# Kernel optimization log

Measured on AMD Instinct MI355X. Metric: run time of the kernel, lower is better.

Reference implementation:

```python
import jax, jax.numpy as jnp
import numpy as np

NEG_FILL = -1e20
SPANS_PER_WORD = 2


def setup_inputs() -> dict:
    key = jax.random.key(0)
    k1, k2, k3, k4, k5 = jax.random.split(key, 5)
    B, N, D, T = 8, 16384, 256, 8
    embeddings = jax.random.normal(k1, (B, N, D), dtype=jnp.float32)
    scores_a = jax.random.normal(k2, (B, N, T), dtype=jnp.float32)
    scores_b = jax.random.normal(k3, (B, N, T), dtype=jnp.float32)
    span_mask = jax.random.randint(k4, (B, N), 0, 2).astype(bool)
    seq_length = jax.random.randint(k5, (B,), 1, 2048).astype(jnp.int32)
    return {
        "embeddings": embeddings,
        "scores_a": scores_a,
        "scores_b": scores_b,
        "span_mask": span_mask,
        "seq_length": seq_length,
    }


def reference(embeddings, scores_a, scores_b, span_mask, seq_length):
    # --- SpanPruner.forward: per-dict-entry softmax, drop null tag, max over tags ---
    probs_list = [jnp.max(jax.nn.softmax(s, axis=2)[:, :, 1:], axis=2)
                  for s in (scores_a, scores_b)]
    probabilities = jnp.maximum(probs_list[0], probs_list[1])  # max over dict entries  [B,N]

    # --- span_pruner ---
    num_keep = jnp.maximum(seq_length * SPANS_PER_WORD, 1)       # [B]
    max_keep = int(jnp.max(num_keep))                            # static k for topk

    scores = jnp.where(span_mask, probabilities, NEG_FILL)       # masked_fill  [B,N]
    _, top_indices = jax.lax.top_k(scores, max_keep)             # [B,K], descending like torch.topk

    top_indices_mask = jnp.arange(max_keep)[None, :] < num_keep[:, None]  # [B,K]
    fill_value = jnp.max(top_indices, axis=1, keepdims=True)
    top_indices = jnp.where(top_indices_mask, top_indices, fill_value)
    top_indices = jnp.sort(top_indices, axis=1)                  # [B,K]

    # batched_index_select gathers
    seq_mask = jnp.take_along_axis(span_mask, top_indices, axis=1)        # [B,K] bool
    top_mask = (top_indices_mask & seq_mask).astype(jnp.int32)            # [B,K]
    top_scores = jnp.take_along_axis(scores, top_indices, axis=1)         # [B,K]
    top_embeddings = jnp.take_along_axis(embeddings, top_indices[:, :, None], axis=1)  # [B,K,D]

    return top_indices, top_embeddings, top_scores, top_mask
```

## Files before the change

### kernel.cpp

```cpp
#include <hip/hip_runtime.h>
#include <math.h>

#define NB 8
#define NN 16384
#define NT 8
#define ND 256
#define NEG_FILL_F (-1e20f)

__device__ __forceinline__ unsigned fkey(float s){
  unsigned u = __float_as_uint(s);
  return (u & 0x80000000u) ? ~u : (u | 0x80000000u);
}
__device__ __forceinline__ float fkey_inv(unsigned k){
  unsigned u = (k & 0x80000000u) ? (k ^ 0x80000000u) : ~k;
  return __uint_as_float(u);
}

__device__ __forceinline__ float prob_of(const float4 x, const float4 y){
  float m = fmaxf(fmaxf(fmaxf(x.x,x.y),fmaxf(x.z,x.w)),
                  fmaxf(fmaxf(y.x,y.y),fmaxf(y.z,y.w)));
  float e0=expf(x.x-m), e1=expf(x.y-m), e2=expf(x.z-m), e3=expf(x.w-m);
  float e4=expf(y.x-m), e5=expf(y.y-m), e6=expf(y.z-m), e7=expf(y.w-m);
  float sum = ((((((e0+e1)+e2)+e3)+e4)+e5)+e6)+e7;
  float pm = fmaxf(fmaxf(fmaxf(e1,e2),fmaxf(e3,e4)),fmaxf(fmaxf(e5,e6),e7));
  return pm/sum;
}

__global__ void k_scores(const float* __restrict__ sa, const float* __restrict__ sb,
                         const int* __restrict__ mask, unsigned* __restrict__ outk,
                         int* __restrict__ gpart){
  __shared__ int lh[256];
  const int t = threadIdx.x;
  lh[t] = 0;
  __syncthreads();
  int i = blockIdx.x*256 + t;
  const float4* pa = (const float4*)(sa + (size_t)i*NT);
  const float4* pb = (const float4*)(sb + (size_t)i*NT);
  float4 a0=pa[0], a1=pa[1], b0=pb[0], b1=pb[1];
  float p = fmaxf(prob_of(a0,a1), prob_of(b0,b1));
  unsigned k = fkey(mask[i] ? p : NEG_FILL_F);
  outk[i] = k;
  atomicAdd(&lh[k>>24], 1);
  __syncthreads();
  gpart[blockIdx.x*256 + t] = lh[t];
}

__device__ int block_scan_excl(int v, int* lds, int tid){
  __syncthreads();
  int lane = tid & 63, wave = tid >> 6;
  int x = v;
  #pragma unroll
  for (int off=1; off<64; off<<=1){
    int y = __shfl_up(x, off, 64);
    if (lane >= off) x += y;
  }
  if (lane == 63) lds[wave] = x;
  __syncthreads();
  if (wave == 0){
    int w = (lane < 16) ? lds[lane] : 0;
    #pragma unroll
    for (int off=1; off<16; off<<=1){
      int y = __shfl_up(w, off, 64);
      if (lane >= off) w += y;
    }
    if (lane < 16) lds[16+lane] = w;
  }
  __syncthreads();
  int waveOff = wave ? lds[16+wave-1] : 0;
  return waveOff + x - v;
}

__device__ void build_hist(const unsigned* kk, unsigned pref, unsigned decided, int shift,
                           unsigned (*whist)[257], int* hist, int tid, int lane, int wave){
  #pragma unroll
  for (int i=0;i<4;++i) whist[wave][lane + 64*i] = 0u;
  __syncthreads();
  #pragma unroll
  for (int j=0;j<16;++j){
    unsigned k = kk[j];
    if (((k ^ pref) & decided) == 0u)
      atomicAdd(&whist[wave][(k>>shift)&255u], 1u);
  }
  __syncthreads();
  if (tid < 256){
    unsigned sum=0;
    #pragma unroll
    for (int w=0;w<16;++w) sum += whist[w][tid];
    hist[tid] = (int)sum;
  }
  __syncthreads();
}

__device__ void scan_pick2(int x, int r0, int r1, bool do1,
                           int* P, int* lds4, int* sOut, int tid, int lane, int wave){
  int Pt = 0;
  if (tid < 256){
    #pragma unroll
    for (int off=1; off<64; off<<=1){
      int y = __shfl_up(x, off, 64);
      if (lane >= off) x += y;
    }
    if (lane==63) lds4[wave] = x;
    Pt = x;
  }
  __syncthreads();
  if (tid < 256){
    int offs = 0;
    for (int w=0; w<wave; ++w) offs += lds4[w];
    Pt += offs;
    P[tid] = Pt;
  }
  __syncthreads();
  if (tid < 256){
    int prev = tid ? P[tid-1] : 0;
    if (Pt >= r0 && prev < r0){ sOut[0] = 255-tid; sOut[1] = r0-prev; }
    if (do1 && Pt >= r1 && prev < r1){ sOut[2] = 255-tid; sOut[3] = r1-prev; }
  }
  __syncthreads();
}

__global__ __launch_bounds__(1024)
void k_select(const unsigned* __restrict__ keys, const int* __restrict__ gpart,
              const int* __restrict__ seq, float* __restrict__ out, int K){
  const int b = blockIdx.x;
  const int tid = threadIdx.x;
  const int lane = tid & 63, wave = tid >> 6;
  __shared__ unsigned whist[16][257];
  __shared__ int part4[4][256];
  __shared__ int hist[256];
  __shared__ int P[256];
  __shared__ int lds[32];
  __shared__ int lds4[4];
  __shared__ int smax[16];
  __shared__ int sOut[4];
  __shared__ int sFill;

  int num_keep = seq[b]*2; if (num_keep < 1) num_keep = 1;

  {
    int grp = tid >> 8;
    int bin = tid & 255;
    const int* gp = gpart + (b*64 + grp*16)*256 + bin;
    int sum = 0;
    #pragma unroll
    for (int w=0; w<16; ++w) sum += gp[w*256];
    part4[grp][bin] = sum;
  }

  const unsigned* kb = keys + (size_t)b*NN + tid*16;
  unsigned kk[16];
  #pragma unroll
  for (int q=0;q<4;++q){
    uint4 v = ((const uint4*)kb)[q];
    kk[4*q+0]=v.x; kk[4*q+1]=v.y; kk[4*q+2]=v.z; kk[4*q+3]=v.w;
  }
  __syncthreads();

  int r0 = K, r1 = num_keep;
  int x0 = 0;
  if (tid < 256){
    int bin = 255 - tid;
    x0 = part4[0][bin] + part4[1][bin] + part4[2][bin] + part4[3][bin];
  }
  scan_pick2(x0, r0, r1, true, P, lds4, sOut, tid, lane, wave);
  unsigned pref0 = (unsigned)sOut[0] << 24;  r0 = sOut[1];
  unsigned pref1 = (unsigned)sOut[2] << 24;  r1 = sOut[3];
  bool same = (pref0 == pref1);
  unsigned decided = 0xFF000000u;
  __syncthreads();

  for (int round=1; round<4; ++round){
    const int shift = 24 - 8*round;
    build_hist(kk, pref0, decided, shift, whist, hist, tid, lane, wave);
    int xv = (tid < 256) ? hist[255-tid] : 0;
    scan_pick2(xv, r0, r1, same, P, lds4, sOut, tid, lane, wave);
    int bin0 = sOut[0], rem0 = sOut[1];
    int bin1 = sOut[2], rem1 = sOut[3];
    __syncthreads();
    if (!same){
      build_hist(kk, pref1, decided, shift, whist, hist, tid, lane, wave);
      int xv1 = (tid < 256) ? hist[255-tid] : 0;
      scan_pick2(xv1, r1, 0, false, P, lds4, sOut, tid, lane, wave);
      bin1 = sOut[0]; rem1 = sOut[1];
      __syncthreads();
    }
    pref0 |= (unsigned)bin0 << shift;  r0 = rem0;
    pref1 |= (unsigned)bin1 << shift;  r1 = rem1;
    same = same && (bin0 == bin1);
    decided |= (0xFFu << shift);
  }
  const unsigned TK = pref0;  const int needK = r0;
  const unsigned TN = pref1;  const int needN = r1;

  int cTK=0, cTN=0;
  #pragma unroll
  for (int j=0;j<16;++j){
    unsigned k = kk[j];
    cTK += (k==TK); cTN += (k==TN);
  }
  int oTK = block_scan_excl(cTK, lds, tid);
  int oTN = block_scan_excl(cTN, lds, tid);

  const int base = tid*16;
  int tK=oTK, tN=oTN, cKept=0, maxIdx=-1;
  #pragma unroll
  for (int j=0;j<16;++j){
    unsigned k=kk[j];
    bool inK  = (k>TK) || ((k==TK) && (tK<needK));  if (k==TK) tK++;
    bool kept = (k>TN) || ((k==TN) && (tN<needN));  if (k==TN) tN++;
    if (inK) maxIdx = base+j;
    cKept += kept;
  }
  int oKept = block_scan_excl(cKept, lds, tid);

  int mv=maxIdx;
  #pragma unroll
  for (int off=32; off; off>>=1){
    int y = __shfl_down(mv, off, 64);
    mv = mv > y ? mv : y;
  }
  if (lane==0) smax[wave]=mv;
  __syncthreads();
  if (tid==0){
    int f=-1;
    for (int i=0;i<16;++i) f = f > smax[i] ? f : smax[i];
    sFill = f;
  }
  __syncthreads();
  const int fill = sFill;

  float* out_idx = out;
  float* out_sc  = out + (size_t)NB*K + (size_t)NB*K*ND;
  float* out_mk  = out_sc + (size_t)NB*K;
  const int ob = b*K;
  const unsigned kNEG = fkey(NEG_FILL_F);

  int tN2=oTN, p=oKept;
  #pragma unroll
  for (int j=0;j<16;++j){
    unsigned k=kk[j];
    bool kept = (k>TN) || ((k==TN) && (tN2<needN));  if (k==TN) tN2++;
    if (kept){
      int n = base+j;
      out_idx[ob+p] = (float)n;
      out_sc[ob+p]  = fkey_inv(k);
      out_mk[ob+p]  = (k != kNEG) ? 1.0f : 0.0f;
      ++p;
    }
  }
  if (num_keep < K){
    float fs = fkey_inv(keys[(size_t)b*NN + fill]);
    for (int q = num_keep + tid; q < K; q += 1024){
      out_idx[ob+q] = (float)fill;
      out_sc[ob+q]  = fs;
      out_mk[ob+q]  = 0.0f;
    }
  }
}

__global__ void k_gather(const float* __restrict__ emb, const float* __restrict__ out_idx,
                         float* __restrict__ out_emb, int K){
  int b = blockIdx.y;
  int g = blockIdx.x*256 + threadIdx.x;
  if (g >= K*64) return;
  int c = g & 63;
  int p = g >> 6;
  size_t r = (size_t)b*K + p;
  int idx = (int)out_idx[r];
  const float4* src = (const float4*)(emb + ((size_t)b*NN + (size_t)idx)*ND);
  float4* dst = (float4*)(out_emb + r*(size_t)ND);
  dst[c] = src[c];
}

extern "C" void kernel_launch(void* const* d_in, const int* in_sizes, int n_in,
                              void* d_out, int out_size, void* d_ws, size_t ws_size,
                              hipStream_t stream) {
  const float* emb  = (const float*)d_in[0];
  const float* sa   = (const float*)d_in[1];
  const float* sb   = (const float*)d_in[2];
  const int*   mask = (const int*)d_in[3];
  const int*   seq  = (const int*)d_in[4];
  float* out = (float*)d_out;
  unsigned* ws_keys = (unsigned*)d_ws;
  int* gpart = (int*)d_ws + (size_t)NB*NN;

  int K = out_size / (NB*(ND+3));
  if (K <= 0) return;

  k_scores<<<(NB*NN)/256, 256, 0, stream>>>(sa, sb, mask, ws_keys, gpart);
  k_select<<<NB, 1024, 0, stream>>>(ws_keys, gpart, seq, out, K);
  dim3 ggrid((K*64 + 255)/256, NB);
  k_gather<<<ggrid, 256, 0, stream>>>(emb, out, out + (size_t)NB*K, K);
}
```

Baseline: 206.8 us.

## Halve select block size, fuse dual radix histograms and packed prefix scans

The per-batch top-k select kernel now runs 512 threads, each holding 32 keys, instead of 1024 threads holding 16. When the two radix thresholds diverge, both histograms are built in a single pass over the keys instead of two. The two exclusive scans for tie counts are packed into one 32-bit scan, and the cross-wave prefix is computed with a simple unrolled sum. Together these cut the number of barriers and LDS passes in a kernel launched with only 8 blocks, at the cost of more registers and less parallelism per block.

```diff
diff --git a/kernel.cpp b/kernel.cpp
--- a/kernel.cpp
+++ b/kernel.cpp
@@ -45,7 +45,7 @@
   gpart[blockIdx.x*256 + t] = lh[t];
 }
 
-__device__ int block_scan_excl(int v, int* lds, int tid){
+__device__ __forceinline__ int block_scan_excl512(int v, int* lds, int tid){
   __syncthreads();
   int lane = tid & 63, wave = tid >> 6;
   int x = v;
@@ -56,45 +56,18 @@
   }
   if (lane == 63) lds[wave] = x;
   __syncthreads();
-  if (wave == 0){
-    int w = (lane < 16) ? lds[lane] : 0;
-    #pragma unroll
-    for (int off=1; off<16; off<<=1){
-      int y = __shfl_up(w, off, 64);
-      if (lane >= off) w += y;
-    }
-    if (lane < 16) lds[16+lane] = w;
-  }
-  __syncthreads();
-  int waveOff = wave ? lds[16+wave-1] : 0;
-  return waveOff + x - v;
-}
-
-__device__ void build_hist(const unsigned* kk, unsigned pref, unsigned decided, int shift,
-                           unsigned (*whist)[257], int* hist, int tid, int lane, int wave){
-  #pragma unroll
-  for (int i=0;i<4;++i) whist[wave][lane + 64*i] = 0u;
-  __syncthreads();
-  #pragma unroll
-  for (int j=0;j<16;++j){
-    unsigned k = kk[j];
-    if (((k ^ pref) & decided) == 0u)
-      atomicAdd(&whist[wave][(k>>shift)&255u], 1u);
-  }
-  __syncthreads();
-  if (tid < 256){
-    unsigned sum=0;
-    #pragma unroll
-    for (int w=0;w<16;++w) sum += whist[w][tid];
-    hist[tid] = (int)sum;
-  }
-  __syncthreads();
-}
-
-__device__ void scan_pick2(int x, int r0, int r1, bool do1,
-                           int* P, int* lds4, int* sOut, int tid, int lane, int wave){
+  int wo = 0;
+  #pragma unroll
+  for (int w=0; w<8; ++w) wo += (w < wave) ? lds[w] : 0;
+  return wo + x - v;
+}
+
+__device__ void scan_pick(const int* hist, int r0, int r1, bool do1,
+                          int* P, int* lds4, int* sOut, int tid, int lane){
   int Pt = 0;
-  if (tid < 256){
+  const int wave = tid >> 6;
+  if (tid < 256){
+    int x = hist[255 - tid];
     #pragma unroll
     for (int off=1; off<64; off<<=1){
       int y = __shfl_up(x, off, 64);
@@ -105,9 +78,10 @@
   }
   __syncthreads();
   if (tid < 256){
-    int offs = 0;
-    for (int w=0; w<wave; ++w) offs += lds4[w];
-    Pt += offs;
+    int wo = 0;
+    #pragma unroll
+    for (int w=0; w<4; ++w) wo += (w < wave) ? lds4[w] : 0;
+    Pt += wo;
     P[tid] = Pt;
   }
   __syncthreads();
@@ -119,20 +93,22 @@
   __syncthreads();
 }
 
-__global__ __launch_bounds__(1024)
+__global__ __launch_bounds__(512, 1)
 void k_select(const unsigned* __restrict__ keys, const int* __restrict__ gpart,
               const int* __restrict__ seq, float* __restrict__ out, int K){
   const int b = blockIdx.x;
   const int tid = threadIdx.x;
   const int lane = tid & 63, wave = tid >> 6;
-  __shared__ unsigned whist[16][257];
-  __shared__ int part4[4][256];
-  __shared__ int hist[256];
+  __shared__ unsigned whA[8][257];
+  __shared__ unsigned whB[8][257];
+  __shared__ int histA[256];
+  __shared__ int histB[256];
   __shared__ int P[256];
-  __shared__ int lds[32];
+  __shared__ int part2[2][256];
+  __shared__ int lds[8];
   __shared__ int lds4[4];
-  __shared__ int smax[16];
-  __shared__ int sOut[4];
+  __shared__ int smax[8];
+  __shared__ int sOut[8];
   __shared__ int sFill;
 
   int num_keep = seq[b]*2; if (num_keep < 1) num_keep = 1;
@@ -140,29 +116,29 @@
   {
     int grp = tid >> 8;
     int bin = tid & 255;
-    const int* gp = gpart + (b*64 + grp*16)*256 + bin;
+    const int* gp = gpart + (b*64 + grp*32)*256 + bin;
     int sum = 0;
     #pragma unroll
-    for (int w=0; w<16; ++w) sum += gp[w*256];
-    part4[grp][bin] = sum;
-  }
-
-  const unsigned* kb = keys + (size_t)b*NN + tid*16;
-  unsigned kk[16];
-  #pragma unroll
-  for (int q=0;q<4;++q){
+    for (int w=0; w<32; ++w) sum += gp[w*256];
+    part2[grp][bin] = sum;
+  }
+
+  const unsigned* kb = keys + (size_t)b*NN + tid*32;
+  unsigned kk[32];
+  #pragma unroll
+  for (int q=0;q<8;++q){
     uint4 v = ((const uint4*)kb)[q];
     kk[4*q+0]=v.x; kk[4*q+1]=v.y; kk[4*q+2]=v.z; kk[4*q+3]=v.w;
   }
   __syncthreads();
 
   int r0 = K, r1 = num_keep;
-  int x0 = 0;
-  if (tid < 256){
-    int bin = 255 - tid;
-    x0 = part4[0][bin] + part4[1][bin] + part4[2][bin] + part4[3][bin];
-  }
-  scan_pick2(x0, r0, r1, true, P, lds4, sOut, tid, lane, wave);
+  if (tid < 256){
+    int bin = tid;
+    histA[bin] = part2[0][bin] + part2[1][bin];
+  }
+  __syncthreads();
+  scan_pick(histA, r0, r1, true, P, lds4, sOut, tid, lane);
   unsigned pref0 = (unsigned)sOut[0] << 24;  r0 = sOut[1];
   unsigned pref1 = (unsigned)sOut[2] << 24;  r1 = sOut[3];
   bool same = (pref0 == pref1);
@@ -171,19 +147,37 @@
 
   for (int round=1; round<4; ++round){
     const int shift = 24 - 8*round;
-    build_hist(kk, pref0, decided, shift, whist, hist, tid, lane, wave);
-    int xv = (tid < 256) ? hist[255-tid] : 0;
-    scan_pick2(xv, r0, r1, same, P, lds4, sOut, tid, lane, wave);
+    #pragma unroll
+    for (int i=0;i<4;++i){
+      whA[wave][lane + 64*i] = 0u;
+      whB[wave][lane + 64*i] = 0u;
+    }
+    __syncthreads();
+    const bool dual = !same;
+    #pragma unroll
+    for (int j=0;j<32;++j){
+      unsigned k = kk[j];
+      if (((k ^ pref0) & decided) == 0u)
+        atomicAdd(&whA[wave][(k>>shift)&255u], 1u);
+      if (dual && ((k ^ pref1) & decided) == 0u)
+        atomicAdd(&whB[wave][(k>>shift)&255u], 1u);
+    }
+    __syncthreads();
+    if (tid < 256){
+      unsigned sa_=0, sb_=0;
+      #pragma unroll
+      for (int w=0;w<8;++w){ sa_ += whA[w][tid]; sb_ += whB[w][tid]; }
+      histA[tid] = (int)sa_;
+      histB[tid] = (int)sb_;
+    }
+    __syncthreads();
+    scan_pick(histA, r0, r1, same, P, lds4, sOut, tid, lane);
+    if (dual)
+      scan_pick(histB, r1, 0, false, P, lds4, sOut+4, tid, lane);
     int bin0 = sOut[0], rem0 = sOut[1];
-    int bin1 = sOut[2], rem1 = sOut[3];
-    __syncthreads();
-    if (!same){
-      build_hist(kk, pref1, decided, shift, whist, hist, tid, lane, wave);
-      int xv1 = (tid < 256) ? hist[255-tid] : 0;
-      scan_pick2(xv1, r1, 0, false, P, lds4, sOut, tid, lane, wave);
-      bin1 = sOut[0]; rem1 = sOut[1];
-      __syncthreads();
-    }
+    int bin1 = dual ? sOut[4] : sOut[2];
+    int rem1 = dual ? sOut[5] : sOut[3];
+    __syncthreads();
     pref0 |= (unsigned)bin0 << shift;  r0 = rem0;
     pref1 |= (unsigned)bin1 << shift;  r1 = rem1;
     same = same && (bin0 == bin1);
@@ -194,24 +188,24 @@
 
   int cTK=0, cTN=0;
   #pragma unroll
-  for (int j=0;j<16;++j){
+  for (int j=0;j<32;++j){
     unsigned k = kk[j];
     cTK += (k==TK); cTN += (k==TN);
   }
-  int oTK = block_scan_excl(cTK, lds, tid);
-  int oTN = block_scan_excl(cTN, lds, tid);
-
-  const int base = tid*16;
+  int packed = block_scan_excl512((cTK<<16)|cTN, lds, tid);
+  int oTK = (packed>>16)&0xFFFF, oTN = packed&0xFFFF;
+
+  const int base = tid*32;
   int tK=oTK, tN=oTN, cKept=0, maxIdx=-1;
   #pragma unroll
-  for (int j=0;j<16;++j){
+  for (int j=0;j<32;++j){
     unsigned k=kk[j];
     bool inK  = (k>TK) || ((k==TK) && (tK<needK));  if (k==TK) tK++;
     bool kept = (k>TN) || ((k==TN) && (tN<needN));  if (k==TN) tN++;
     if (inK) maxIdx = base+j;
     cKept += kept;
   }
-  int oKept = block_scan_excl(cKept, lds, tid);
+  int oKept = block_scan_excl512(cKept, lds, tid);
 
   int mv=maxIdx;
   #pragma unroll
@@ -223,7 +217,8 @@
   __syncthreads();
   if (tid==0){
     int f=-1;
-    for (int i=0;i<16;++i) f = f > smax[i] ? f : smax[i];
+    #pragma unroll
+    for (int i=0;i<8;++i) f = f > smax[i] ? f : smax[i];
     sFill = f;
   }
   __syncthreads();
@@ -237,7 +232,7 @@
 
   int tN2=oTN, p=oKept;
   #pragma unroll
-  for (int j=0;j<16;++j){
+  for (int j=0;j<32;++j){
     unsigned k=kk[j];
     bool kept = (k>TN) || ((k==TN) && (tN2<needN));  if (k==TN) tN2++;
     if (kept){
@@ -250,7 +245,7 @@
   }
   if (num_keep < K){
     float fs = fkey_inv(keys[(size_t)b*NN + fill]);
-    for (int q = num_keep + tid; q < K; q += 1024){
+    for (int q = num_keep + tid; q < K; q += 512){
       out_idx[ob+q] = (float)fill;
       out_sc[ob+q]  = fs;
       out_mk[ob+q]  = 0.0f;
@@ -288,7 +283,7 @@
   if (K <= 0) return;
 
   k_scores<<<(NB*NN)/256, 256, 0, stream>>>(sa, sb, mask, ws_keys, gpart);
-  k_select<<<NB, 1024, 0, stream>>>(ws_keys, gpart, seq, out, K);
+  k_select<<<NB, 512, 0, stream>>>(ws_keys, gpart, seq, out, K);
   dim3 ggrid((K*64 + 255)/256, NB);
   k_gather<<<ggrid, 256, 0, stream>>>(emb, out, out + (size_t)NB*K, K);
 }
```

New measurement: 210.3 us. About the same (+1.7%).
